# Kernel optimization log

Measured on AMD Instinct MI355X. Metric: run time of the kernel, lower is better.

Reference implementation:

```python
import jax, jax.numpy as jnp
import numpy as np

MEM, W, K = 65536, 128, 8
R = K + 1  # sparse reads + last-used slot
B, IN = 32, 512
IFACE = 2 * W + R + 1  # 266


def setup_inputs() -> dict:
    key = jax.random.key(0)
    ks = jax.random.split(key, 8)
    return {
        "x": jax.random.normal(ks[0], (B, IN), jnp.float32),
        "W_if": jax.random.normal(ks[1], (IN, IFACE), jnp.float32) * 0.02,
        "b_if": jnp.zeros((IFACE,), jnp.float32),
        "memory": jax.random.normal(ks[2], (B, MEM, W), jnp.float32),
        "read_weights": jax.random.uniform(ks[3], (B, 1, R), jnp.float32),
        "read_vectors": jax.random.normal(ks[4], (B, R, W), jnp.float32),
        "read_positions": jax.random.randint(ks[5], (B, R), 0, MEM, jnp.int32),
        "last_used_mem": jax.random.randint(ks[6], (B, 1), 0, MEM, jnp.int32),
    }


def reference(x, W_if, b_if, memory, read_weights, read_vectors, read_positions, last_used_mem):
    b = x.shape[0]
    # interface projection (independent_linears=False path)
    xi = x @ W_if + b_if                                   # (b, 2w+r+1)
    read_query = xi[:, :W]                                  # (b, w)
    write_vector = xi[:, W:2 * W][:, None, :]               # (b, 1, w)
    gate = jax.nn.sigmoid(xi[:, 2 * W:2 * W + R])[:, None, :]  # (b, 1, r)
    write_gate = jax.nn.sigmoid(xi[:, -1])[:, None, None]   # (b, 1, 1)
    # write: interpolate read weights, outer-product update of read vectors
    write_weights = write_gate * (gate * read_weights + (1.0 - gate))  # (b,1,r)
    new_rv = read_vectors + jnp.einsum('bkr,bkw->brw', write_weights, write_vector)  # (b,r,w)
    # write_into_sparse_memory: scatter read vectors into previous read positions
    brange = jnp.arange(b)[:, None]
    memory = memory.at[brange, read_positions].set(new_rv)
    # read: exact KNN (replaces CPU KD-tree search): squared L2 to all cells
    d2 = (jnp.sum(memory * memory, axis=-1)
          - 2.0 * jnp.einsum('bmw,bw->bm', memory, read_query)
          + jnp.sum(read_query * read_query, axis=-1, keepdims=True))  # (b, m)
    _, pos = jax.lax.top_k(-d2, K)                          # K nearest positions
    positions = jnp.concatenate([jnp.clip(pos, 0, MEM - 1), last_used_mem], axis=1)  # (b, r)
    gathered = jnp.take_along_axis(memory, positions[:, :, None], axis=1)  # (b, r, w)
    return gathered[:, :-1, :]  # (b, K, w) — forward output of read()
```

## Files before the change

### kernel.cpp

```cpp
#include <hip/hip_runtime.h>
#include <float.h>
#include <limits.h>

#define MEMN 65536
#define WD 128
#define KSEL 8
#define RD 9
#define BD 32
#define IND 512
#define IFACE 266
#define XI_STRIDE 272

#define KSEG 8
#define KSEG_LEN (IND / KSEG)

#define NCHUNK 64
#define ROWS_PER_CHUNK 1024
#define CAND_SCAN (NCHUNK * KSEL)
#define CAND_REAL (CAND_SCAN + RD)
#define CAND_PER_BATCH 528

typedef float fvec4 __attribute__((ext_vector_type(4)));

#define TOP8_INSERT(bv, bi, vin, iin)                                  \
  { float _v = (vin); int _i = (iin);                                  \
    _Pragma("unroll")                                                  \
    for (int _j = 0; _j < 8; ++_j) {                                   \
      bool _b = (_v < bv[_j]) || (_v == bv[_j] && _i < bi[_j]);        \
      float _tv = bv[_j]; int _ti = bi[_j];                            \
      bv[_j] = _b ? _v : _tv;  bi[_j] = _b ? _i : _ti;                 \
      _v = _b ? _tv : _v;      _i = _b ? _ti : _i;                     \
    } }

__device__ __forceinline__ fvec4 ntload(const void* p) {
  return __builtin_nontemporal_load((const fvec4*)p);
}

__global__ __launch_bounds__(288)
void xi_part_kernel(const float* __restrict__ x, const float* __restrict__ Wif,
                    float* __restrict__ xi_part) {
  const int b = blockIdx.x, seg = blockIdx.y, c = threadIdx.x;
  if (c >= IFACE) return;
  const float* xr = x + b * IND + seg * KSEG_LEN;
  const float* wp = Wif + (size_t)(seg * KSEG_LEN) * IFACE + c;
  float a0 = 0.f, a1 = 0.f, a2 = 0.f, a3 = 0.f;
  #pragma unroll
  for (int k = 0; k < KSEG_LEN; k += 4) {
    a0 += xr[k]     * wp[(size_t)k * IFACE];
    a1 += xr[k + 1] * wp[(size_t)(k + 1) * IFACE];
    a2 += xr[k + 2] * wp[(size_t)(k + 2) * IFACE];
    a3 += xr[k + 3] * wp[(size_t)(k + 3) * IFACE];
  }
  xi_part[(b * KSEG + seg) * XI_STRIDE + c] = (a0 + a1) + (a2 + a3);
}

__global__ __launch_bounds__(320)
void head_kernel(const float* __restrict__ xi_part, const float* __restrict__ bif,
                 const float* __restrict__ read_weights, const float* __restrict__ read_vectors,
                 const int* __restrict__ rpos,
                 float* __restrict__ xi, float* __restrict__ new_rv,
                 float* __restrict__ cand_val, int* __restrict__ cand_idx) {
  const int b = blockIdx.x, t = threadIdx.x;
  __shared__ float xiS[IFACE];
  __shared__ float wwS[RD];
  __shared__ float nvS[RD][WD];

  if (t < IFACE) {
    float acc = bif[t];
    #pragma unroll
    for (int s = 0; s < KSEG; ++s)
      acc += xi_part[(b * KSEG + s) * XI_STRIDE + t];
    xiS[t] = acc;
    xi[b * XI_STRIDE + t] = acc;
  }
  __syncthreads();

  if (t < RD) {
    float g  = 1.f / (1.f + __expf(-xiS[2 * WD + t]));
    float wg = 1.f / (1.f + __expf(-xiS[IFACE - 1]));
    wwS[t] = wg * (g * read_weights[b * RD + t] + (1.f - g));
  }
  __syncthreads();

  if (t < WD) {
    const float wv = xiS[WD + t];
    #pragma unroll
    for (int r = 0; r < RD; ++r) {
      float nv = read_vectors[(b * RD + r) * WD + t] + wwS[r] * wv;
      nvS[r][t] = nv;
      new_rv[(b * RD + r) * WD + t] = nv;
    }
  }
  __syncthreads();

  if (t < 64) {
    const int lane = t;
    const float q0 = xiS[lane * 2], q1 = xiS[lane * 2 + 1];
    for (int r = 0; r < RD; ++r) {
      float m0 = nvS[r][lane * 2], m1 = nvS[r][lane * 2 + 1];
      float s = m0 * (m0 - 2.f * q0) + m1 * (m1 - 2.f * q1);
      #pragma unroll
      for (int off = 32; off; off >>= 1) s += __shfl_xor(s, off);
      if (lane == 0) {
        int p = rpos[b * RD + r];
        bool dup = false;
        for (int r2 = r + 1; r2 < RD; ++r2) dup |= (rpos[b * RD + r2] == p);
        int slot = b * CAND_PER_BATCH + CAND_SCAN + r;
        cand_val[slot] = dup ? FLT_MAX : s;
        cand_idx[slot] = dup ? INT_MAX : p;
      }
    }
  }
}

__global__ __launch_bounds__(256)
void scan_kernel(const float* __restrict__ memory, const float* __restrict__ xi,
                 const int* __restrict__ rpos,
                 float* __restrict__ cand_val, int* __restrict__ cand_idx) {
  const int b = blockIdx.y, chunk = blockIdx.x;
  const int t = threadIdx.x;
  const int w = t >> 6, l = t & 63, g = l >> 2, ln = l & 3;

  int rp[RD];
  #pragma unroll
  for (int r = 0; r < RD; ++r) rp[r] = rpos[b * RD + r];

  fvec4 tq[8];
  #pragma unroll
  for (int j = 0; j < 8; ++j) {
    fvec4 q = *(const fvec4*)(xi + b * XI_STRIDE + j * 16 + ln * 4);
    tq[j] = q * 2.f;
  }

  float bv[8]; int bi[8];
  #pragma unroll
  for (int j = 0; j < 8; ++j) { bv[j] = FLT_MAX; bi[j] = INT_MAX; }

  const char* memB = (const char*)memory + (size_t)b * MEMN * (WD * 4);

  #pragma unroll 2
  for (int i = 0; i < ROWS_PER_CHUNK / 64; ++i) {
    const int m = (i * NCHUNK + chunk) * 64 + w * 16 + g;
    const char* p = memB + (size_t)m * (WD * 4) + ln * 16;
    float sA = 0.f, sB = 0.f;
    #pragma unroll
    for (int j = 0; j < 8; j += 2) {
      fvec4 m0 = ntload(p + j * 64);
      fvec4 m1 = ntload(p + (j + 1) * 64);
      sA += m0.x * (m0.x - tq[j].x) + m0.y * (m0.y - tq[j].y)
          + m0.z * (m0.z - tq[j].z) + m0.w * (m0.w - tq[j].w);
      sB += m1.x * (m1.x - tq[j + 1].x) + m1.y * (m1.y - tq[j + 1].y)
          + m1.z * (m1.z - tq[j + 1].z) + m1.w * (m1.w - tq[j + 1].w);
    }
    float s = sA + sB;
    s += __shfl_xor(s, 1);
    s += __shfl_xor(s, 2);
    if (ln == 0) {
      bool skip = false;
      #pragma unroll
      for (int r = 0; r < RD; ++r) skip |= (m == rp[r]);
      if (!skip && (s < bv[7] || (s == bv[7] && m < bi[7]))) TOP8_INSERT(bv, bi, s, m);
    }
  }

  __shared__ float lv[64][8];
  __shared__ int   li[64][8];
  if (ln == 0) {
    #pragma unroll
    for (int j = 0; j < 8; ++j) { lv[w * 16 + g][j] = bv[j]; li[w * 16 + g][j] = bi[j]; }
  }
  __syncthreads();
  for (int s = 32; s >= 1; s >>= 1) {
    if (t < s) {
      float mv[8]; int mi[8];
      #pragma unroll
      for (int j = 0; j < 8; ++j) { mv[j] = lv[t][j]; mi[j] = li[t][j]; }
      #pragma unroll
      for (int j = 0; j < 8; ++j) {
        float v = lv[t + s][j]; int i = li[t + s][j];
        if (v < mv[7] || (v == mv[7] && i < mi[7])) TOP8_INSERT(mv, mi, v, i);
      }
      #pragma unroll
      for (int j = 0; j < 8; ++j) { lv[t][j] = mv[j]; li[t][j] = mi[j]; }
    }
    __syncthreads();
  }
  if (t < 8) {
    cand_val[b * CAND_PER_BATCH + chunk * 8 + t] = lv[0][t];
    cand_idx[b * CAND_PER_BATCH + chunk * 8 + t] = li[0][t];
  }
}

__global__ __launch_bounds__(128)
void final_kernel(const float* __restrict__ cand_val, const int* __restrict__ cand_idx,
                  const float* __restrict__ memory, const float* __restrict__ new_rv,
                  const int* __restrict__ rpos, float* __restrict__ out) {
  const int b = blockIdx.x, t = threadIdx.x;
  __shared__ float lv[128][8];
  __shared__ int   li[128][8];
  __shared__ int   posS[KSEL], srcS[KSEL];

  float bv[8]; int bi[8];
  #pragma unroll
  for (int j = 0; j < 8; ++j) { bv[j] = FLT_MAX; bi[j] = INT_MAX; }

  for (int e = t; e < CAND_REAL; e += 128) {
    float v = cand_val[b * CAND_PER_BATCH + e];
    int   i = cand_idx[b * CAND_PER_BATCH + e];
    if (v < bv[7] || (v == bv[7] && i < bi[7])) TOP8_INSERT(bv, bi, v, i);
  }
  #pragma unroll
  for (int j = 0; j < 8; ++j) { lv[t][j] = bv[j]; li[t][j] = bi[j]; }
  __syncthreads();

  for (int stride = 64; stride >= 1; stride >>= 1) {
    if (t < stride) {
      #pragma unroll
      for (int j = 0; j < 8; ++j) {
        float v = lv[t + stride][j]; int i = li[t + stride][j];
        if (v < bv[7] || (v == bv[7] && i < bi[7])) TOP8_INSERT(bv, bi, v, i);
      }
      #pragma unroll
      for (int j = 0; j < 8; ++j) { lv[t][j] = bv[j]; li[t][j] = bi[j]; }
    }
    __syncthreads();
  }

  if (t < KSEL) {
    int p = li[0][t];
    int src = -1;
    for (int r = 0; r < RD; ++r) if (rpos[b * RD + r] == p) src = r;
    posS[t] = p; srcS[t] = src;
  }
  __syncthreads();

  for (int e = t; e < KSEL * WD; e += 128) {
    int k = e >> 7, wv = e & 127;
    int p = posS[k], src = srcS[k];
    float val = (src >= 0) ? new_rv[(b * RD + src) * WD + wv]
                           : memory[((size_t)b * MEMN + p) * WD + wv];
    out[b * KSEL * WD + e] = val;
  }
}

extern "C" void kernel_launch(void* const* d_in, const int* in_sizes, int n_in,
                              void* d_out, int out_size, void* d_ws, size_t ws_size,
                              hipStream_t stream) {
  const float* x      = (const float*)d_in[0];
  const float* Wif    = (const float*)d_in[1];
  const float* bif    = (const float*)d_in[2];
  const float* memory = (const float*)d_in[3];
  const float* rw     = (const float*)d_in[4];
  const float* rv     = (const float*)d_in[5];
  const int*   rpos   = (const int*)d_in[6];

  float* ws       = (float*)d_ws;
  float* xi_part  = ws;
  float* xi       = xi_part + BD * KSEG * XI_STRIDE;
  float* new_rv   = xi + BD * XI_STRIDE;
  float* cand_val = new_rv + BD * RD * WD;
  int*   cand_idx = (int*)(cand_val + BD * CAND_PER_BATCH);
  float* out      = (float*)d_out;

  xi_part_kernel<<<dim3(BD, KSEG), dim3(288), 0, stream>>>(x, Wif, xi_part);
  head_kernel<<<dim3(BD), dim3(320), 0, stream>>>(xi_part, bif, rw, rv, rpos,
                                                  xi, new_rv, cand_val, cand_idx);
  scan_kernel<<<dim3(NCHUNK, BD), dim3(256), 0, stream>>>(memory, xi, rpos, cand_val, cand_idx);
  final_kernel<<<dim3(BD), dim3(128), 0, stream>>>(cand_val, cand_idx, memory, new_rv, rpos, out);
}
```

Baseline: 240.7 us.

## Remap scan to contiguous per-wave row blocks with 8 lanes per row

The scan kernel now gives each wave a contiguous 256-row slice of its chunk instead of interleaving rows across chunks. Each row is read by 8 lanes, each loading four 16-byte vectors, so every wave load covers 8 whole consecutive rows (4 KB contiguous). It adds one extra shuffle step to the reduction and halves the per-block candidate lists in the shared-memory merge. Goals are more sequential DRAM access per wave and less per-lane register and top-8 bookkeeping, at the cost of fewer independent top-8 lists and one more shuffle per row.

```diff
diff --git a/kernel.cpp b/kernel.cpp
--- a/kernel.cpp
+++ b/kernel.cpp
@@ -119,16 +119,17 @@
                  float* __restrict__ cand_val, int* __restrict__ cand_idx) {
   const int b = blockIdx.y, chunk = blockIdx.x;
   const int t = threadIdx.x;
-  const int w = t >> 6, l = t & 63, g = l >> 2, ln = l & 3;
+  const int w = t >> 6, l = t & 63, g = l >> 3, ln = l & 7;
+  const int waveBase = chunk * ROWS_PER_CHUNK + w * (ROWS_PER_CHUNK / 4);
 
   int rp[RD];
   #pragma unroll
   for (int r = 0; r < RD; ++r) rp[r] = rpos[b * RD + r];
 
-  fvec4 tq[8];
-  #pragma unroll
-  for (int j = 0; j < 8; ++j) {
-    fvec4 q = *(const fvec4*)(xi + b * XI_STRIDE + j * 16 + ln * 4);
+  fvec4 tq[4];
+  #pragma unroll
+  for (int j = 0; j < 4; ++j) {
+    fvec4 q = *(const fvec4*)(xi + b * XI_STRIDE + j * 32 + ln * 4);
     tq[j] = q * 2.f;
   }
 
@@ -136,26 +137,32 @@
   #pragma unroll
   for (int j = 0; j < 8; ++j) { bv[j] = FLT_MAX; bi[j] = INT_MAX; }
 
-  const char* memB = (const char*)memory + (size_t)b * MEMN * (WD * 4);
+  const char* base = (const char*)memory + (size_t)b * MEMN * (WD * 4)
+                   + (size_t)(waveBase + g) * (WD * 4) + ln * 16;
 
   #pragma unroll 2
-  for (int i = 0; i < ROWS_PER_CHUNK / 64; ++i) {
-    const int m = (i * NCHUNK + chunk) * 64 + w * 16 + g;
-    const char* p = memB + (size_t)m * (WD * 4) + ln * 16;
-    float sA = 0.f, sB = 0.f;
-    #pragma unroll
-    for (int j = 0; j < 8; j += 2) {
-      fvec4 m0 = ntload(p + j * 64);
-      fvec4 m1 = ntload(p + (j + 1) * 64);
-      sA += m0.x * (m0.x - tq[j].x) + m0.y * (m0.y - tq[j].y)
-          + m0.z * (m0.z - tq[j].z) + m0.w * (m0.w - tq[j].w);
-      sB += m1.x * (m1.x - tq[j + 1].x) + m1.y * (m1.y - tq[j + 1].y)
-          + m1.z * (m1.z - tq[j + 1].z) + m1.w * (m1.w - tq[j + 1].w);
-    }
+  for (int i = 0; i < ROWS_PER_CHUNK / 4 / 8; ++i) {
+    const char* p = base + (size_t)i * 4096;
+    const fvec4 m0 = ntload(p);
+    const fvec4 m1 = ntload(p + 128);
+    const fvec4 m2 = ntload(p + 256);
+    const fvec4 m3 = ntload(p + 384);
+
+    float sA = m0.x*(m0.x-tq[0].x) + m0.y*(m0.y-tq[0].y)
+             + m0.z*(m0.z-tq[0].z) + m0.w*(m0.w-tq[0].w)
+             + m1.x*(m1.x-tq[1].x) + m1.y*(m1.y-tq[1].y)
+             + m1.z*(m1.z-tq[1].z) + m1.w*(m1.w-tq[1].w);
+    float sB = m2.x*(m2.x-tq[2].x) + m2.y*(m2.y-tq[2].y)
+             + m2.z*(m2.z-tq[2].z) + m2.w*(m2.w-tq[2].w)
+             + m3.x*(m3.x-tq[3].x) + m3.y*(m3.y-tq[3].y)
+             + m3.z*(m3.z-tq[3].z) + m3.w*(m3.w-tq[3].w);
     float s = sA + sB;
     s += __shfl_xor(s, 1);
     s += __shfl_xor(s, 2);
+    s += __shfl_xor(s, 4);
+
     if (ln == 0) {
+      const int m = waveBase + i * 8 + g;
       bool skip = false;
       #pragma unroll
       for (int r = 0; r < RD; ++r) skip |= (m == rp[r]);
@@ -163,14 +170,14 @@
     }
   }
 
-  __shared__ float lv[64][8];
-  __shared__ int   li[64][8];
+  __shared__ float lv[32][8];
+  __shared__ int   li[32][8];
   if (ln == 0) {
     #pragma unroll
-    for (int j = 0; j < 8; ++j) { lv[w * 16 + g][j] = bv[j]; li[w * 16 + g][j] = bi[j]; }
-  }
-  __syncthreads();
-  for (int s = 32; s >= 1; s >>= 1) {
+    for (int j = 0; j < 8; ++j) { lv[w * 8 + g][j] = bv[j]; li[w * 8 + g][j] = bi[j]; }
+  }
+  __syncthreads();
+  for (int s = 16; s >= 1; s >>= 1) {
     if (t < s) {
       float mv[8]; int mi[8];
       #pragma unroll
```

New measurement: 227.8 us. -5.4%, faster.
